# Optimization experiments

Measured on AMD Instinct MI355X. Metric: run time of the kernel, lower is better.

The kernel has to match this reference:

```python
import jax, jax.numpy as jnp
import numpy as np

T, H, I, E, TOPK = 4096, 2048, 4096, 8, 2


def setup_inputs() -> dict:
    key = jax.random.key(0)
    k0, k1, k2, k3, k4, k5 = jax.random.split(key, 6)
    return {
        "hidden_states": jax.random.normal(k0, (T, H), dtype=jnp.float32),
        "expert_affinities": jax.random.uniform(k1, (T, E), dtype=jnp.float32),
        "expert_index": jax.random.randint(k2, (T, TOPK), 0, E),
        "w_gate": jax.random.normal(k3, (E, H, I), dtype=jnp.float32) / np.float32(np.sqrt(H)),
        "w_up": jax.random.normal(k4, (E, H, I), dtype=jnp.float32) / np.float32(np.sqrt(H)),
        "w_down": jax.random.normal(k5, (E, I, H), dtype=jnp.float32) / np.float32(np.sqrt(I)),
    }


def reference(hidden_states, expert_affinities, expert_index, w_gate, w_up, w_down):
    num_experts = w_gate.shape[0]
    # top_k-hot mask (T, E); duplicate expert picks accumulate, matching torch loop
    expert_mask = jnp.sum(jax.nn.one_hot(expert_index, num_experts, dtype=jnp.float32), axis=1)
    # mask affinities to chosen experts, then L1-normalize (F.normalize p=1, eps=1e-12)
    aff = jnp.where(expert_mask == 0, 0.0, expert_affinities)
    aff = aff / jnp.maximum(jnp.sum(jnp.abs(aff), axis=1, keepdims=True), 1e-12)
    # all-experts GLU MLP: every expert processes all tokens
    g = jnp.einsum('th,ehi->eti', hidden_states, w_gate)   # (E, T, I)
    u = jnp.einsum('th,ehi->eti', hidden_states, w_up)     # (E, T, I)
    h = jax.nn.silu(g) * u                                  # (E, T, I)
    out_e = jnp.einsum('eti,eih->eth', h, w_down)           # (E, T, H)
    # affinity-weighted combine across experts
    return jnp.einsum('eth,te->th', out_e, aff)             # (T, H)
```

## Files before the change

### kernel.cpp

```cpp
#include <hip/hip_runtime.h>
#include <hip/hip_bf16.h>


constexpr int kT   = 4096;
constexpr int kH   = 2048;
constexpr int kI   = 4096;
constexpr int kE   = 8;
constexpr int kCap = 4096;
constexpr int kRowsCap = 10240;

typedef __attribute__((ext_vector_type(8))) short bf16x8;
typedef __attribute__((ext_vector_type(4))) float f32x4;

constexpr size_t HSB_OFF  = 0;
constexpr size_t HBUF_OFF = 16777216;
constexpr size_t RA_OFF   = HBUF_OFF + (size_t)kRowsCap * kI * 2;
constexpr size_t RB_OFF   = RA_OFF + (size_t)kE * kH * kI * 2;
constexpr size_t CNT_OFF  = RB_OFF + (size_t)kE * kH * kI * 2;
constexpr size_t OFF_OFF  = CNT_OFF + 256;
constexpr size_t LTOK_OFF = OFF_OFF + 256;
constexpr size_t LW_OFF   = LTOK_OFF + (size_t)kE * kCap * 4;
constexpr size_t POS_OFF  = LW_OFF + (size_t)kE * kCap * 4;
constexpr size_t WROW_OFF = POS_OFF + (size_t)kT * 2 * 4;

__device__ __forceinline__ unsigned short f2bf(float x) {
  unsigned int u = __float_as_uint(x);
  u += 0x7FFFu + ((u >> 16) & 1u);
  return (unsigned short)(u >> 16);
}
__device__ __forceinline__ unsigned pk2(float a, float b) {
  return (unsigned)f2bf(a) | ((unsigned)f2bf(b) << 16);
}
__device__ __forceinline__ float silu_f(float x) { return x / (1.f + __expf(-x)); }

__device__ __forceinline__ void async_copy16(void* lds, const void* g) {
  __builtin_amdgcn_global_load_lds(
      (const __attribute__((address_space(1))) void*)g,
      (__attribute__((address_space(3))) void*)lds, 16, 0, 0);
}

#define MFMA_BF16 __builtin_amdgcn_mfma_f32_16x16x32_bf16

__global__ void cvt_hs_kernel(const float* __restrict__ in, unsigned short* __restrict__ out) {
  size_t i = ((size_t)blockIdx.x * 256 + threadIdx.x) * 8;
  float4 a = *(const float4*)(in + i);
  float4 b = *(const float4*)(in + i + 4);
  uint4 v;
  v.x = pk2(a.x, a.y); v.y = pk2(a.z, a.w);
  v.z = pk2(b.x, b.y); v.w = pk2(b.z, b.w);
  *(uint4*)(out + i) = v;
}

__global__ __launch_bounds__(256)
void tcvt_kernel(const float* __restrict__ src, unsigned short* __restrict__ dst,
                 int K, int N) {
  __shared__ __attribute__((aligned(16))) unsigned short s[64][72];
  const size_t mat = (size_t)K * N;
  const float* S = src + (size_t)blockIdx.z * mat;
  unsigned short* D = dst + (size_t)blockIdx.z * mat;
  const int k0 = blockIdx.y * 64, n0 = blockIdx.x * 64;
  const int t  = threadIdx.x;
  const int n4 = (t & 15) * 4;
  const int k4 = (t >> 4) * 4;
  const float* p0 = S + (size_t)(k0 + k4) * N + n0 + n4;
  float4 r0 = *(const float4*)(p0);
  float4 r1 = *(const float4*)(p0 + N);
  float4 r2 = *(const float4*)(p0 + 2 * (size_t)N);
  float4 r3 = *(const float4*)(p0 + 3 * (size_t)N);
  uint2 v;
  v.x = pk2(r0.x, r1.x); v.y = pk2(r2.x, r3.x); *(uint2*)(&s[n4 + 0][k4]) = v;
  v.x = pk2(r0.y, r1.y); v.y = pk2(r2.y, r3.y); *(uint2*)(&s[n4 + 1][k4]) = v;
  v.x = pk2(r0.z, r1.z); v.y = pk2(r2.z, r3.z); *(uint2*)(&s[n4 + 2][k4]) = v;
  v.x = pk2(r0.w, r1.w); v.y = pk2(r2.w, r3.w); *(uint2*)(&s[n4 + 3][k4]) = v;
  __syncthreads();
  const int nn = t >> 3;
  const int kc = (t & 7) * 8;
#pragma unroll
  for (int i = 0; i < 2; ++i) {
    const int n = nn + i * 32;
    uint4 u = *(const uint4*)(&s[n][kc]);
    *(uint4*)(D + (size_t)(n0 + n) * K + k0 + kc) = u;
  }
}

__global__ void route_kernel(const float* __restrict__ aff, const int* __restrict__ idx,
                             int* counts, int* ltok, float* lw, int* pos) {
  int t = blockIdx.x * 256 + threadIdx.x;
  if (t >= kT) return;
  int e0 = idx[t * 2 + 0];
  int e1 = idx[t * 2 + 1];
  float a0 = aff[t * kE + e0];
  float a1 = aff[t * kE + e1];
  if (e0 == e1) {
    float w = a0 / fmaxf(fabsf(a0), 1e-12f);
    int s = atomicAdd(&counts[e0], 1);
    ltok[e0 * kCap + s] = t;
    lw[e0 * kCap + s]   = w;
    pos[t * 2 + 0] = (e0 << 12) | s;
    pos[t * 2 + 1] = -1;
  } else {
    float d = fmaxf(fabsf(a0) + fabsf(a1), 1e-12f);
    int s0 = atomicAdd(&counts[e0], 1);
    ltok[e0 * kCap + s0] = t;
    lw[e0 * kCap + s0]   = a0 / d;
    int s1 = atomicAdd(&counts[e1], 1);
    ltok[e1 * kCap + s1] = t;
    lw[e1 * kCap + s1]   = a1 / d;
    pos[t * 2 + 0] = (e0 << 12) | s0;
    pos[t * 2 + 1] = (e1 << 12) | s1;
  }
}

__global__ void prefix_kernel(const int* __restrict__ counts, int* offs) {
  if (threadIdx.x == 0 && blockIdx.x == 0) {
    int acc = 0;
    for (int e = 0; e < kE; ++e) { offs[e] = acc; acc += (counts[e] + 255) & ~255; }
  }
}

__global__ void wrow_kernel(const int* __restrict__ counts, const int* __restrict__ offs,
                            const float* __restrict__ lw, float* __restrict__ wrow) {
  int idx = blockIdx.x * 256 + threadIdx.x;
  int e = idx >> 12, s = idx & 4095;
  int cnt = counts[e];
  int al  = (cnt + 255) & ~255;
  if (s < al) wrow[offs[e] + s] = (s < cnt) ? lw[e * kCap + s] : 0.f;
}

__global__ __launch_bounds__(512, 2)
void gemm_gu_kernel(const unsigned short* __restrict__ hsb,
                    const unsigned short* __restrict__ wgT,
                    const unsigned short* __restrict__ wuT,
                    const int* __restrict__ counts, const int* __restrict__ offs,
                    const int* __restrict__ ltok, const float* __restrict__ wrow,
                    unsigned short* __restrict__ hbuf) {
  constexpr int S = kH / 32;
  __shared__ __attribute__((aligned(16))) unsigned short lds[4 * 16384];

  const int e   = blockIdx.z;
  const int cnt = counts[e];
  const int m0  = blockIdx.y * 256;
  if (m0 >= cnt) return;
  const int n0   = blockIdx.x * 128;
  const int tid  = threadIdx.x;
  const int lane = tid & 63;
  const int wv   = tid >> 6;
  const int wm   = wv >> 2;
  const int wn   = wv & 3;
  const int baseRow = offs[e] + m0;

  const int skof = ((tid & 3) ^ ((tid >> 3) & 3)) * 8;
  int sl0 = m0 + (tid >> 2);        sl0 = sl0 < cnt ? sl0 : cnt - 1;
  int sl1 = m0 + 128 + (tid >> 2);  sl1 = sl1 < cnt ? sl1 : cnt - 1;
  const unsigned short* aP0 = hsb + (size_t)ltok[e * kCap + sl0] * kH + skof;
  const unsigned short* aP1 = hsb + (size_t)ltok[e * kCap + sl1] * kH + skof;
  const unsigned short* wgP = wgT + (size_t)e * kI * kH
                                  + (size_t)(n0 + (tid >> 2)) * kH + skof;
  const unsigned short* wuP = wuT + (size_t)e * kI * kH
                                  + (size_t)(n0 + (tid >> 2)) * kH + skof;
  char* ldsb = (char*)lds;
  const int aO0 = tid * 16;
  const int aO1 = aO0 + 8192;
  const int wO  = tid * 16;

#define GU_STG_A(s) { const int sb_ = ((s) & 3) * 32768; const int ko_ = (s) * 32;  \
    async_copy16(ldsb + sb_ + aO0, aP0 + ko_);                                      \
    async_copy16(ldsb + sb_ + aO1, aP1 + ko_); }
#define GU_STG_W(s) { const int sb_ = ((s) & 3) * 32768; const int ko_ = (s) * 32;  \
    async_copy16(ldsb + sb_ + 16384 + wO, wgP + ko_);                               \
    async_copy16(ldsb + sb_ + 24576 + wO, wuP + ko_); }

  f32x4 accG[8][2] = {};
  f32x4 accU[8][2] = {};
  const int ar = lane & 15;
  const int fo = (((lane >> 4) ^ ((lane >> 1) & 3)) << 4);

#define GU_SLICE(s, STG, VM)                                                         \
  {                                                                                  \
    const char* sb = ldsb + ((s) & 3) * 32768;                                       \
    if (STG) { GU_STG_A((s) + 3); GU_STG_W((s) + 3); }                               \
    bf16x8 fA[8], fWg[2], fWu[2];                                                    \
    _Pragma("unroll") for (int mf = 0; mf < 8; ++mf)                                 \
      fA[mf] = *(const bf16x8*)(sb + (wm * 128 + mf * 16 + ar) * 64 + fo);           \
    _Pragma("unroll") for (int nf = 0; nf < 2; ++nf) {                               \
      fWg[nf] = *(const bf16x8*)(sb + 16384 + (wn * 32 + nf * 16 + ar) * 64 + fo);   \
      fWu[nf] = *(const bf16x8*)(sb + 24576 + (wn * 32 + nf * 16 + ar) * 64 + fo);   \
    }                                                                                \
    __builtin_amdgcn_s_setprio(1);                                                   \
    _Pragma("unroll") for (int mf = 0; mf < 8; ++mf)                                 \
      _Pragma("unroll") for (int nf = 0; nf < 2; ++nf) {                             \
        accG[mf][nf] = MFMA_BF16(fWg[nf], fA[mf], accG[mf][nf], 0, 0, 0);            \
        accU[mf][nf] = MFMA_BF16(fWu[nf], fA[mf], accU[mf][nf], 0, 0, 0);            \
      }                                                                              \
    __builtin_amdgcn_s_setprio(0);                                                   \
    if ((VM) >= 0) {                                                                 \
      asm volatile("s_waitcnt vmcnt(%0)" :: "i"((VM) < 0 ? 0 : (VM)) : "memory");    \
      __builtin_amdgcn_s_barrier();                                                  \
    }                                                                                \
  }

  GU_STG_A(0); GU_STG_W(0);
  GU_STG_A(1); GU_STG_W(1);
  GU_STG_A(2); GU_STG_W(2);
  asm volatile("s_waitcnt vmcnt(8)" ::: "memory");
  __builtin_amdgcn_s_barrier();

  for (int s = 0; s < S - 3; ++s) GU_SLICE(s, true, 8);
  GU_SLICE(S - 3, false, 4);
  GU_SLICE(S - 2, false, 0);
  GU_SLICE(S - 1, false, -1);
#undef GU_SLICE
#undef GU_STG_A
#undef GU_STG_W

  const int lr4 = (lane >> 4) * 4;
#pragma unroll
  for (int mf = 0; mf < 8; ++mf) {
    const int grow = baseRow + wm * 128 + mf * 16 + ar;
    const float wf = wrow[grow];
#pragma unroll
    for (int nf = 0; nf < 2; ++nf) {
      const int n = n0 + wn * 32 + nf * 16 + lr4;
      f32x4 g = accG[mf][nf], u = accU[mf][nf];
      float h0 = silu_f(g[0]) * u[0] * wf;
      float h1 = silu_f(g[1]) * u[1] * wf;
      float h2 = silu_f(g[2]) * u[2] * wf;
      float h3 = silu_f(g[3]) * u[3] * wf;
      uint2 v;
      v.x = pk2(h0, h1);
      v.y = pk2(h2, h3);
      *(uint2*)(hbuf + ((size_t)grow * kI + n)) = v;
    }
  }
}

__global__ __launch_bounds__(512, 2)
void gemm_dn_kernel(const unsigned short* __restrict__ hbuf,
                    const unsigned short* __restrict__ wdT,
                    const int* __restrict__ counts, const int* __restrict__ offs,
                    float* __restrict__ obuf) {
  constexpr int S = kI / 32;
  __shared__ __attribute__((aligned(16))) unsigned short lds[4 * 16384];

  const int e   = blockIdx.z;
  const int cnt = counts[e];
  const int m0  = blockIdx.y * 256;
  if (m0 >= cnt) return;
  const int n0   = blockIdx.x * 256;
  const int tid  = threadIdx.x;
  const int lane = tid & 63;
  const int wv   = tid >> 6;
  const int wm   = wv >> 2;
  const int wn   = wv & 3;
  const int baseRow = offs[e] + m0;

  const int skof = ((tid & 3) ^ ((tid >> 3) & 3)) * 8;
  const unsigned short* aP0 = hbuf + (size_t)(baseRow + (tid >> 2)) * kI + skof;
  const unsigned short* aP1 = hbuf + (size_t)(baseRow + 128 + (tid >> 2)) * kI + skof;
  const unsigned short* wP0 = wdT + (size_t)e * kH * kI
                                  + (size_t)(n0 + (tid >> 2)) * kI + skof;
  const unsigned short* wP1 = wdT + (size_t)e * kH * kI
                                  + (size_t)(n0 + 128 + (tid >> 2)) * kI + skof;
  char* ldsb = (char*)lds;
  const int cO0 = tid * 16;
  const int cO1 = cO0 + 8192;

#define DN_STG_A(s) { const int sb_ = ((s) & 3) * 32768; const int ko_ = (s) * 32;  \
    async_copy16(ldsb + sb_ + cO0, aP0 + ko_);                                      \
    async_copy16(ldsb + sb_ + cO1, aP1 + ko_); }
#define DN_STG_W(s) { const int sb_ = ((s) & 3) * 32768; const int ko_ = (s) * 32;  \
    async_copy16(ldsb + sb_ + 16384 + cO0, wP0 + ko_);                              \
    async_copy16(ldsb + sb_ + 16384 + cO1, wP1 + ko_); }

  f32x4 acc[8][4] = {};
  const int ar = lane & 15;
  const int fo = (((lane >> 4) ^ ((lane >> 1) & 3)) << 4);

#define DN_SLICE(s, STG, VM)                                                         \
  {                                                                                  \
    const char* sb = ldsb + ((s) & 3) * 32768;                                       \
    if (STG) { DN_STG_A((s) + 3); DN_STG_W((s) + 3); }                               \
    bf16x8 fA[8], fW[4];                                                             \
    _Pragma("unroll") for (int mf = 0; mf < 8; ++mf)                                 \
      fA[mf] = *(const bf16x8*)(sb + (wm * 128 + mf * 16 + ar) * 64 + fo);           \
    _Pragma("unroll") for (int nf = 0; nf < 4; ++nf)                                 \
      fW[nf] = *(const bf16x8*)(sb + 16384 + (wn * 64 + nf * 16 + ar) * 64 + fo);    \
    __builtin_amdgcn_s_setprio(1);                                                   \
    _Pragma("unroll") for (int mf = 0; mf < 8; ++mf)                                 \
      _Pragma("unroll") for (int nf = 0; nf < 4; ++nf)                               \
        acc[mf][nf] = MFMA_BF16(fW[nf], fA[mf], acc[mf][nf], 0, 0, 0);               \
    __builtin_amdgcn_s_setprio(0);                                                   \
    if ((VM) >= 0) {                                                                 \
      asm volatile("s_waitcnt vmcnt(%0)" :: "i"((VM) < 0 ? 0 : (VM)) : "memory");    \
      __builtin_amdgcn_s_barrier();                                                  \
    }                                                                                \
  }

  DN_STG_A(0); DN_STG_W(0);
  DN_STG_A(1); DN_STG_W(1);
  DN_STG_A(2); DN_STG_W(2);
  asm volatile("s_waitcnt vmcnt(8)" ::: "memory");
  __builtin_amdgcn_s_barrier();

  for (int s = 0; s < S - 3; ++s) DN_SLICE(s, true, 8);
  DN_SLICE(S - 3, false, 4);
  DN_SLICE(S - 2, false, 0);
  DN_SLICE(S - 1, false, -1);
#undef DN_SLICE
#undef DN_STG_A
#undef DN_STG_W

  const int lr4 = (lane >> 4) * 4;
#pragma unroll
  for (int mf = 0; mf < 8; ++mf) {
    const int grow = baseRow + wm * 128 + mf * 16 + ar;
#pragma unroll
    for (int nf = 0; nf < 4; ++nf) {
      const int n = n0 + wn * 64 + nf * 16 + lr4;
      *(f32x4*)(obuf + (size_t)grow * kH + n) = acc[mf][nf];
    }
  }
}

__global__ void combine_kernel(const float* __restrict__ obuf,
                               const int* __restrict__ pos,
                               const int* __restrict__ offs,
                               float* __restrict__ out) {
  const int t   = blockIdx.y;
  const int col = blockIdx.x * 1024 + threadIdx.x * 4;
  const int c0  = pos[t * 2 + 0];
  const int c1  = pos[t * 2 + 1];
  const int row0 = offs[c0 >> 12] + (c0 & 4095);
  float4 v = *(const float4*)(obuf + (size_t)row0 * kH + col);
  if (c1 >= 0) {
    const int row1 = offs[c1 >> 12] + (c1 & 4095);
    float4 w = *(const float4*)(obuf + (size_t)row1 * kH + col);
    v.x += w.x; v.y += w.y; v.z += w.z; v.w += w.w;
  }
  *(float4*)(out + (size_t)t * kH + col) = v;
}

extern "C" void kernel_launch(void* const* d_in, const int* in_sizes, int n_in,
                              void* d_out, int out_size, void* d_ws, size_t ws_size,
                              hipStream_t stream) {
  const float* hs   = (const float*)d_in[0];
  const float* aff  = (const float*)d_in[1];
  const int*   eidx = (const int*)d_in[2];
  const float* wg   = (const float*)d_in[3];
  const float* wu   = (const float*)d_in[4];
  const float* wd   = (const float*)d_in[5];
  float* out = (float*)d_out;

  char* ws = (char*)d_ws;
  unsigned short* hsb  = (unsigned short*)(ws + HSB_OFF);
  unsigned short* hbuf = (unsigned short*)(ws + HBUF_OFF);
  unsigned short* wgT  = (unsigned short*)(ws + RA_OFF);
  unsigned short* wdT  = (unsigned short*)(ws + RA_OFF);
  unsigned short* wuT  = (unsigned short*)(ws + RB_OFF);
  float*          obuf = (float*)(ws + RB_OFF);
  int*            cnts = (int*)(ws + CNT_OFF);
  int*            offs = (int*)(ws + OFF_OFF);
  int*            ltok = (int*)(ws + LTOK_OFF);
  float*          lwgt = (float*)(ws + LW_OFF);
  int*            pos  = (int*)(ws + POS_OFF);
  float*          wrow = (float*)(ws + WROW_OFF);

  hipMemsetAsync(cnts, 0, kE * sizeof(int), stream);

  cvt_hs_kernel<<<(kT * kH) / (256 * 8), 256, 0, stream>>>(hs, hsb);
  route_kernel<<<kT / 256, 256, 0, stream>>>(aff, eidx, cnts, ltok, lwgt, pos);
  prefix_kernel<<<1, 64, 0, stream>>>(cnts, offs);
  wrow_kernel<<<(kE * kCap) / 256, 256, 0, stream>>>(cnts, offs, lwgt, wrow);

  tcvt_kernel<<<dim3(kI / 64, kH / 64, kE), 256, 0, stream>>>(wg, wgT, kH, kI);
  tcvt_kernel<<<dim3(kI / 64, kH / 64, kE), 256, 0, stream>>>(wu, wuT, kH, kI);

  gemm_gu_kernel<<<dim3(kI / 128, kCap / 256, kE), 512, 0, stream>>>(
      hsb, wgT, wuT, cnts, offs, ltok, wrow, hbuf);

  tcvt_kernel<<<dim3(kH / 64, kI / 64, kE), 256, 0, stream>>>(wd, wdT, kI, kH);

  gemm_dn_kernel<<<dim3(kH / 256, kCap / 256, kE), 512, 0, stream>>>(
      hbuf, wdT, cnts, offs, obuf);

  combine_kernel<<<dim3(kH / 1024, kT), 256, 0, stream>>>(obuf, pos, offs, out);
}
```

Baseline: 775.9 us.

## Double-buffer A-fragment LDS reads across K slices in GEMM kernels

Both grouped GEMM kernels now read the next slice's activation fragments from LDS into a second register set while the current slice's MFMAs run, ping-ponging between two register arrays. To make the next buffer ready one slice early, the global-load waits are tightened to leave fewer copies in flight (vmcnt 4 instead of 8), and an lgkmcnt(0) wait is added before each barrier. This hides LDS read latency behind matrix math, at the cost of more vector registers (which may lower occupancy) and a shallower effective prefetch depth for global loads. The loop is unrolled by two and assumes S is even and at least 4.

```diff
diff --git a/kernel.cpp b/kernel.cpp
--- a/kernel.cpp
+++ b/kernel.cpp
@@ -175,26 +175,29 @@
   const int ar = lane & 15;
   const int fo = (((lane >> 4) ^ ((lane >> 1) & 3)) << 4);
 
-#define GU_SLICE(s, STG, VM)                                                         \
+#define GU_BODY(s, CUR, NXT, STG, RD, VM)                                            \
   {                                                                                  \
-    const char* sb = ldsb + ((s) & 3) * 32768;                                       \
+    const char* sbc = ldsb + ((s) & 3) * 32768;                                      \
+    const char* sbn = ldsb + (((s) + 1) & 3) * 32768;                                \
     if (STG) { GU_STG_A((s) + 3); GU_STG_W((s) + 3); }                               \
-    bf16x8 fA[8], fWg[2], fWu[2];                                                    \
-    _Pragma("unroll") for (int mf = 0; mf < 8; ++mf)                                 \
-      fA[mf] = *(const bf16x8*)(sb + (wm * 128 + mf * 16 + ar) * 64 + fo);           \
+    bf16x8 wg_[2], wu_[2];                                                           \
     _Pragma("unroll") for (int nf = 0; nf < 2; ++nf) {                               \
-      fWg[nf] = *(const bf16x8*)(sb + 16384 + (wn * 32 + nf * 16 + ar) * 64 + fo);   \
-      fWu[nf] = *(const bf16x8*)(sb + 24576 + (wn * 32 + nf * 16 + ar) * 64 + fo);   \
+      wg_[nf] = *(const bf16x8*)(sbc + 16384 + (wn * 32 + nf * 16 + ar) * 64 + fo);  \
+      wu_[nf] = *(const bf16x8*)(sbc + 24576 + (wn * 32 + nf * 16 + ar) * 64 + fo);  \
+    }                                                                                \
+    if (RD) {                                                                        \
+      _Pragma("unroll") for (int mf = 0; mf < 8; ++mf)                               \
+        NXT[mf] = *(const bf16x8*)(sbn + (wm * 128 + mf * 16 + ar) * 64 + fo);       \
     }                                                                                \
     __builtin_amdgcn_s_setprio(1);                                                   \
     _Pragma("unroll") for (int mf = 0; mf < 8; ++mf)                                 \
       _Pragma("unroll") for (int nf = 0; nf < 2; ++nf) {                             \
-        accG[mf][nf] = MFMA_BF16(fWg[nf], fA[mf], accG[mf][nf], 0, 0, 0);            \
-        accU[mf][nf] = MFMA_BF16(fWu[nf], fA[mf], accU[mf][nf], 0, 0, 0);            \
+        accG[mf][nf] = MFMA_BF16(wg_[nf], CUR[mf], accG[mf][nf], 0, 0, 0);           \
+        accU[mf][nf] = MFMA_BF16(wu_[nf], CUR[mf], accU[mf][nf], 0, 0, 0);           \
       }                                                                              \
     __builtin_amdgcn_s_setprio(0);                                                   \
     if ((VM) >= 0) {                                                                 \
-      asm volatile("s_waitcnt vmcnt(%0)" :: "i"((VM) < 0 ? 0 : (VM)) : "memory");    \
+      asm volatile("s_waitcnt vmcnt(%0) lgkmcnt(0)" :: "i"((VM) < 0 ? 0 : (VM)) : "memory"); \
       __builtin_amdgcn_s_barrier();                                                  \
     }                                                                                \
   }
@@ -202,14 +205,23 @@
   GU_STG_A(0); GU_STG_W(0);
   GU_STG_A(1); GU_STG_W(1);
   GU_STG_A(2); GU_STG_W(2);
-  asm volatile("s_waitcnt vmcnt(8)" ::: "memory");
+  asm volatile("s_waitcnt vmcnt(4)" ::: "memory");
   __builtin_amdgcn_s_barrier();
 
-  for (int s = 0; s < S - 3; ++s) GU_SLICE(s, true, 8);
-  GU_SLICE(S - 3, false, 4);
-  GU_SLICE(S - 2, false, 0);
-  GU_SLICE(S - 1, false, -1);
-#undef GU_SLICE
+  bf16x8 aA[8], aB[8];
+#pragma unroll
+  for (int mf = 0; mf < 8; ++mf)
+    aA[mf] = *(const bf16x8*)(ldsb + (wm * 128 + mf * 16 + ar) * 64 + fo);
+
+  for (int s = 0; s < S - 4; s += 2) {
+    GU_BODY(s,     aA, aB, 1, 1, 4);
+    GU_BODY(s + 1, aB, aA, 1, 1, 4);
+  }
+  GU_BODY(S - 4, aA, aB, 1, 1, 4);
+  GU_BODY(S - 3, aB, aA, 0, 1, 0);
+  GU_BODY(S - 2, aA, aB, 0, 1, -1);
+  GU_BODY(S - 1, aB, aA, 0, 0, -1);
+#undef GU_BODY
 #undef GU_STG_A
 #undef GU_STG_W
 
@@ -276,22 +288,25 @@
   const int ar = lane & 15;
   const int fo = (((lane >> 4) ^ ((lane >> 1) & 3)) << 4);
 
-#define DN_SLICE(s, STG, VM)                                                         \
+#define DN_BODY(s, CUR, NXT, STG, RD, VM)                                            \
   {                                                                                  \
-    const char* sb = ldsb + ((s) & 3) * 32768;                                       \
+    const char* sbc = ldsb + ((s) & 3) * 32768;                                      \
+    const char* sbn = ldsb + (((s) + 1) & 3) * 32768;                                \
     if (STG) { DN_STG_A((s) + 3); DN_STG_W((s) + 3); }                               \
-    bf16x8 fA[8], fW[4];                                                             \
-    _Pragma("unroll") for (int mf = 0; mf < 8; ++mf)                                 \
-      fA[mf] = *(const bf16x8*)(sb + (wm * 128 + mf * 16 + ar) * 64 + fo);           \
+    bf16x8 fW[4];                                                                    \
     _Pragma("unroll") for (int nf = 0; nf < 4; ++nf)                                 \
-      fW[nf] = *(const bf16x8*)(sb + 16384 + (wn * 64 + nf * 16 + ar) * 64 + fo);    \
+      fW[nf] = *(const bf16x8*)(sbc + 16384 + (wn * 64 + nf * 16 + ar) * 64 + fo);   \
+    if (RD) {                                                                        \
+      _Pragma("unroll") for (int mf = 0; mf < 8; ++mf)                               \
+        NXT[mf] = *(const bf16x8*)(sbn + (wm * 128 + mf * 16 + ar) * 64 + fo);       \
+    }                                                                                \
     __builtin_amdgcn_s_setprio(1);                                                   \
     _Pragma("unroll") for (int mf = 0; mf < 8; ++mf)                                 \
       _Pragma("unroll") for (int nf = 0; nf < 4; ++nf)                               \
-        acc[mf][nf] = MFMA_BF16(fW[nf], fA[mf], acc[mf][nf], 0, 0, 0);               \
+        acc[mf][nf] = MFMA_BF16(fW[nf], CUR[mf], acc[mf][nf], 0, 0, 0);              \
     __builtin_amdgcn_s_setprio(0);                                                   \
     if ((VM) >= 0) {                                                                 \
-      asm volatile("s_waitcnt vmcnt(%0)" :: "i"((VM) < 0 ? 0 : (VM)) : "memory");    \
+      asm volatile("s_waitcnt vmcnt(%0) lgkmcnt(0)" :: "i"((VM) < 0 ? 0 : (VM)) : "memory"); \
       __builtin_amdgcn_s_barrier();                                                  \
     }                                                                                \
   }
@@ -299,14 +314,23 @@
   DN_STG_A(0); DN_STG_W(0);
   DN_STG_A(1); DN_STG_W(1);
   DN_STG_A(2); DN_STG_W(2);
-  asm volatile("s_waitcnt vmcnt(8)" ::: "memory");
+  asm volatile("s_waitcnt vmcnt(4)" ::: "memory");
   __builtin_amdgcn_s_barrier();
 
-  for (int s = 0; s < S - 3; ++s) DN_SLICE(s, true, 8);
-  DN_SLICE(S - 3, false, 4);
-  DN_SLICE(S - 2, false, 0);
-  DN_SLICE(S - 1, false, -1);
-#undef DN_SLICE
+  bf16x8 aA[8], aB[8];
+#pragma unroll
+  for (int mf = 0; mf < 8; ++mf)
+    aA[mf] = *(const bf16x8*)(ldsb + (wm * 128 + mf * 16 + ar) * 64 + fo);
+
+  for (int s = 0; s < S - 4; s += 2) {
+    DN_BODY(s,     aA, aB, 1, 1, 4);
+    DN_BODY(s + 1, aB, aA, 1, 1, 4);
+  }
+  DN_BODY(S - 4, aA, aB, 1, 1, 4);
+  DN_BODY(S - 3, aB, aA, 0, 1, 0);
+  DN_BODY(S - 2, aA, aB, 0, 1, -1);
+  DN_BODY(S - 1, aB, aA, 0, 0, -1);
+#undef DN_BODY
 #undef DN_STG_A
 #undef DN_STG_W
 
```

Result: no change. 774.9 us (-0.1%).

## Restructure MoE GEMMs to double-buffered 64-wide K tiles with ping-pong barrier schedule

Applied to the files above, without the earlier changes.

Both the gate/up and down-projection GEMM kernels switch from a 4-stage ring of 32-wide K slices to two 64-wide K-tile buffers. Each tile is split into four MFMA quarter phases separated by barriers, with global-to-LDS async copies for later tiles issued between phases. The LDS swizzle is widened to 8 chunks and the warp-to-row mapping changes to two 128-row halves. The aim is to halve the waitcnt/barrier overhead per K unit and interleave loads with MFMA work more finely, at the cost of more barriers per tile and shallower prefetch depth.

```diff
diff --git a/kernel.cpp b/kernel.cpp
--- a/kernel.cpp
+++ b/kernel.cpp
@@ -134,8 +134,8 @@
                     const int* __restrict__ counts, const int* __restrict__ offs,
                     const int* __restrict__ ltok, const float* __restrict__ wrow,
                     unsigned short* __restrict__ hbuf) {
-  constexpr int S = kH / 32;
-  __shared__ __attribute__((aligned(16))) unsigned short lds[4 * 16384];
+  constexpr int NT = kH / 64;
+  __shared__ __attribute__((aligned(16))) unsigned short lds[2 * 32768];
 
   const int e   = blockIdx.z;
   const int cnt = counts[e];
@@ -149,89 +149,127 @@
   const int wn   = wv & 3;
   const int baseRow = offs[e] + m0;
 
-  const int skof = ((tid & 3) ^ ((tid >> 3) & 3)) * 8;
-  int sl0 = m0 + (tid >> 2);        sl0 = sl0 < cnt ? sl0 : cnt - 1;
-  int sl1 = m0 + 128 + (tid >> 2);  sl1 = sl1 < cnt ? sl1 : cnt - 1;
-  const unsigned short* aP0 = hsb + (size_t)ltok[e * kCap + sl0] * kH + skof;
-  const unsigned short* aP1 = hsb + (size_t)ltok[e * kCap + sl1] * kH + skof;
-  const unsigned short* wgP = wgT + (size_t)e * kI * kH
-                                  + (size_t)(n0 + (tid >> 2)) * kH + skof;
-  const unsigned short* wuP = wuT + (size_t)e * kI * kH
-                                  + (size_t)(n0 + (tid >> 2)) * kH + skof;
+  const int skof = ((tid & 7) ^ ((tid >> 3) & 7)) * 8;
+  const int r_   = tid >> 3;
+  int s0 = m0 + r_;        s0 = s0 < cnt ? s0 : cnt - 1;
+  int s1 = m0 + 64 + r_;   s1 = s1 < cnt ? s1 : cnt - 1;
+  int s2 = m0 + 128 + r_;  s2 = s2 < cnt ? s2 : cnt - 1;
+  int s3 = m0 + 192 + r_;  s3 = s3 < cnt ? s3 : cnt - 1;
+  const unsigned short* aP0 = hsb + (size_t)ltok[e * kCap + s0] * kH + skof;
+  const unsigned short* aP1 = hsb + (size_t)ltok[e * kCap + s1] * kH + skof;
+  const unsigned short* aP2 = hsb + (size_t)ltok[e * kCap + s2] * kH + skof;
+  const unsigned short* aP3 = hsb + (size_t)ltok[e * kCap + s3] * kH + skof;
+  const unsigned short* wgP0 = wgT + (size_t)e * kI * kH + (size_t)(n0 + r_) * kH + skof;
+  const unsigned short* wgP1 = wgT + (size_t)e * kI * kH + (size_t)(n0 + 64 + r_) * kH + skof;
+  const unsigned short* wuP0 = wuT + (size_t)e * kI * kH + (size_t)(n0 + r_) * kH + skof;
+  const unsigned short* wuP1 = wuT + (size_t)e * kI * kH + (size_t)(n0 + 64 + r_) * kH + skof;
+
   char* ldsb = (char*)lds;
-  const int aO0 = tid * 16;
-  const int aO1 = aO0 + 8192;
-  const int wO  = tid * 16;
-
-#define GU_STG_A(s) { const int sb_ = ((s) & 3) * 32768; const int ko_ = (s) * 32;  \
-    async_copy16(ldsb + sb_ + aO0, aP0 + ko_);                                      \
-    async_copy16(ldsb + sb_ + aO1, aP1 + ko_); }
-#define GU_STG_W(s) { const int sb_ = ((s) & 3) * 32768; const int ko_ = (s) * 32;  \
-    async_copy16(ldsb + sb_ + 16384 + wO, wgP + ko_);                               \
-    async_copy16(ldsb + sb_ + 24576 + wO, wuP + ko_); }
+  const int stO0 = tid * 16;
+  const int stO1 = tid * 16 + 8192;
+  const int ar  = lane & 15;
+  const int lg  = lane >> 4;
+  const int sk0 = ((lg ^ (lane & 7)) << 4);
+  const int sk1 = (((4 + lg) ^ (lane & 7)) << 4);
 
   f32x4 accG[8][2] = {};
   f32x4 accU[8][2] = {};
-  const int ar = lane & 15;
-  const int fo = (((lane >> 4) ^ ((lane >> 1) & 3)) << 4);
-
-#define GU_SLICE(s, STG, VM)                                                         \
-  {                                                                                  \
-    const char* sb = ldsb + ((s) & 3) * 32768;                                       \
-    if (STG) { GU_STG_A((s) + 3); GU_STG_W((s) + 3); }                               \
-    bf16x8 fA[8], fWg[2], fWu[2];                                                    \
-    _Pragma("unroll") for (int mf = 0; mf < 8; ++mf)                                 \
-      fA[mf] = *(const bf16x8*)(sb + (wm * 128 + mf * 16 + ar) * 64 + fo);           \
-    _Pragma("unroll") for (int nf = 0; nf < 2; ++nf) {                               \
-      fWg[nf] = *(const bf16x8*)(sb + 16384 + (wn * 32 + nf * 16 + ar) * 64 + fo);   \
-      fWu[nf] = *(const bf16x8*)(sb + 24576 + (wn * 32 + nf * 16 + ar) * 64 + fo);   \
-    }                                                                                \
-    __builtin_amdgcn_s_setprio(1);                                                   \
-    _Pragma("unroll") for (int mf = 0; mf < 8; ++mf)                                 \
-      _Pragma("unroll") for (int nf = 0; nf < 2; ++nf) {                             \
-        accG[mf][nf] = MFMA_BF16(fWg[nf], fA[mf], accG[mf][nf], 0, 0, 0);            \
-        accU[mf][nf] = MFMA_BF16(fWu[nf], fA[mf], accU[mf][nf], 0, 0, 0);            \
-      }                                                                              \
-    __builtin_amdgcn_s_setprio(0);                                                   \
-    if ((VM) >= 0) {                                                                 \
-      asm volatile("s_waitcnt vmcnt(%0)" :: "i"((VM) < 0 ? 0 : (VM)) : "memory");    \
-      __builtin_amdgcn_s_barrier();                                                  \
-    }                                                                                \
-  }
-
-  GU_STG_A(0); GU_STG_W(0);
-  GU_STG_A(1); GU_STG_W(1);
-  GU_STG_A(2); GU_STG_W(2);
-  asm volatile("s_waitcnt vmcnt(8)" ::: "memory");
-  __builtin_amdgcn_s_barrier();
-
-  for (int s = 0; s < S - 3; ++s) GU_SLICE(s, true, 8);
-  GU_SLICE(S - 3, false, 4);
-  GU_SLICE(S - 2, false, 0);
-  GU_SLICE(S - 1, false, -1);
-#undef GU_SLICE
-#undef GU_STG_A
-#undef GU_STG_W
-
-  const int lr4 = (lane >> 4) * 4;
-#pragma unroll
-  for (int mf = 0; mf < 8; ++mf) {
-    const int grow = baseRow + wm * 128 + mf * 16 + ar;
-    const float wf = wrow[grow];
-#pragma unroll
-    for (int nf = 0; nf < 2; ++nf) {
-      const int n = n0 + wn * 32 + nf * 16 + lr4;
-      f32x4 g = accG[mf][nf], u = accU[mf][nf];
-      float h0 = silu_f(g[0]) * u[0] * wf;
-      float h1 = silu_f(g[1]) * u[1] * wf;
-      float h2 = silu_f(g[2]) * u[2] * wf;
-      float h3 = silu_f(g[3]) * u[3] * wf;
-      uint2 v;
-      v.x = pk2(h0, h1);
-      v.y = pk2(h2, h3);
-      *(uint2*)(hbuf + ((size_t)grow * kI + n)) = v;
+  bf16x8 a0[4][2], a1[4][2], wgf[2][2], wuf[2][2];
+
+#define STG2(dst, p0, p1, tt) {                                   \
+    async_copy16((dst) + stO0, (p0) + (size_t)(tt) * 64);         \
+    async_copy16((dst) + stO1, (p1) + (size_t)(tt) * 64); }
+#define RD_A(dst, base, mh) _Pragma("unroll")                                  \
+  for (int mf = 0; mf < 4; ++mf) {                                             \
+    const char* rp_ = (base) + ((mh) * 128 + wm * 64 + mf * 16 + ar) * 128;    \
+    dst[mf][0] = *(const bf16x8*)(rp_ + sk0);                                  \
+    dst[mf][1] = *(const bf16x8*)(rp_ + sk1); }
+#define RD_W(dst, base) _Pragma("unroll")                                      \
+  for (int nf = 0; nf < 2; ++nf) {                                             \
+    const char* rp_ = (base) + (wn * 32 + nf * 16 + ar) * 128;                 \
+    dst[nf][0] = *(const bf16x8*)(rp_ + sk0);                                  \
+    dst[nf][1] = *(const bf16x8*)(rp_ + sk1); }
+#define MMA16(ACC, W, A, MH)                                                   \
+  __builtin_amdgcn_s_setprio(1);                                               \
+  _Pragma("unroll") for (int mf = 0; mf < 4; ++mf)                             \
+    _Pragma("unroll") for (int nf = 0; nf < 2; ++nf) {                         \
+      ACC[(MH)*4+mf][nf] = MFMA_BF16(W[nf][0], A[mf][0], ACC[(MH)*4+mf][nf], 0, 0, 0); \
+      ACC[(MH)*4+mf][nf] = MFMA_BF16(W[nf][1], A[mf][1], ACC[(MH)*4+mf][nf], 0, 0, 0); \
+    }                                                                          \
+  __builtin_amdgcn_s_setprio(0);
+
+#define GU_TILE(t, SA1, SM, VM)                                                \
+  {                                                                            \
+    char* bc = ldsb + ((t) & 1) * 65536;                                       \
+    char* bo = ldsb + (((t) + 1) & 1) * 65536;                                 \
+    RD_A(a0, bc, 0); RD_W(wgf, bc + 32768);                                    \
+    if (SA1) STG2(bo + 16384, aP2, aP3, (t) + 1);                              \
+    __builtin_amdgcn_s_barrier();                                              \
+    MMA16(accG, wgf, a0, 0);                                                   \
+    __builtin_amdgcn_s_barrier();                                              \
+    RD_W(wuf, bc + 49152);                                                     \
+    if (SM) STG2(bc, aP0, aP1, (t) + 2);                                       \
+    __builtin_amdgcn_s_barrier();                                              \
+    MMA16(accU, wuf, a0, 0);                                                   \
+    __builtin_amdgcn_s_barrier();                                              \
+    RD_A(a1, bc, 1);                                                           \
+    if (SM) STG2(bc + 32768, wgP0, wgP1, (t) + 2);                             \
+    __builtin_amdgcn_s_barrier();                                              \
+    MMA16(accG, wgf, a1, 1);                                                   \
+    __builtin_amdgcn_s_barrier();                                              \
+    if (SM) STG2(bc + 49152, wuP0, wuP1, (t) + 2);                             \
+    __builtin_amdgcn_s_barrier();                                              \
+    MMA16(accU, wuf, a1, 1);                                                   \
+    if ((VM) >= 0) {                                                           \
+      asm volatile("s_waitcnt vmcnt(%0)" :: "i"((VM) < 0 ? 0 : (VM)) : "memory"); \
+      __builtin_amdgcn_s_barrier();                                            \
+    }                                                                          \
+  }
+
+  {
+    char* b0 = ldsb;
+    char* b1 = ldsb + 65536;
+    STG2(b0,         aP0, aP1, 0);
+    STG2(b0 + 16384, aP2, aP3, 0);
+    STG2(b0 + 32768, wgP0, wgP1, 0);
+    STG2(b0 + 49152, wuP0, wuP1, 0);
+    STG2(b1,         aP0, aP1, 1);
+    STG2(b1 + 32768, wgP0, wgP1, 1);
+    STG2(b1 + 49152, wuP0, wuP1, 1);
+    asm volatile("s_waitcnt vmcnt(6)" ::: "memory");
+    __builtin_amdgcn_s_barrier();
+  }
+
+  for (int t = 0; t < NT - 2; ++t) GU_TILE(t, 1, 1, 6);
+  GU_TILE(NT - 2, 1, 0, 0);
+  GU_TILE(NT - 1, 0, 0, -1);
+#undef GU_TILE
+
+  const int lr4 = lg * 4;
+#pragma unroll
+  for (int mh = 0; mh < 2; ++mh)
+#pragma unroll
+    for (int mf = 0; mf < 4; ++mf) {
+      const int grow = baseRow + mh * 128 + wm * 64 + mf * 16 + ar;
+      const float wf = wrow[grow];
+#pragma unroll
+      for (int nf = 0; nf < 2; ++nf) {
+        const int n = n0 + wn * 32 + nf * 16 + lr4;
+        f32x4 g = accG[mh * 4 + mf][nf], u = accU[mh * 4 + mf][nf];
+        float h0 = silu_f(g[0]) * u[0] * wf;
+        float h1 = silu_f(g[1]) * u[1] * wf;
+        float h2 = silu_f(g[2]) * u[2] * wf;
+        float h3 = silu_f(g[3]) * u[3] * wf;
+        uint2 v;
+        v.x = pk2(h0, h1);
+        v.y = pk2(h2, h3);
+        *(uint2*)(hbuf + ((size_t)grow * kI + n)) = v;
+      }
     }
-  }
+#undef STG2
+#undef RD_A
+#undef RD_W
+#undef MMA16
 }
 
 __global__ __launch_bounds__(512, 2)
@@ -239,8 +277,8 @@
                     const unsigned short* __restrict__ wdT,
                     const int* __restrict__ counts, const int* __restrict__ offs,
                     float* __restrict__ obuf) {
-  constexpr int S = kI / 32;
-  __shared__ __attribute__((aligned(16))) unsigned short lds[4 * 16384];
+  constexpr int NT = kI / 64;
+  __shared__ __attribute__((aligned(16))) unsigned short lds[2 * 32768];
 
   const int e   = blockIdx.z;
   const int cnt = counts[e];
@@ -254,72 +292,116 @@
   const int wn   = wv & 3;
   const int baseRow = offs[e] + m0;
 
-  const int skof = ((tid & 3) ^ ((tid >> 3) & 3)) * 8;
-  const unsigned short* aP0 = hbuf + (size_t)(baseRow + (tid >> 2)) * kI + skof;
-  const unsigned short* aP1 = hbuf + (size_t)(baseRow + 128 + (tid >> 2)) * kI + skof;
-  const unsigned short* wP0 = wdT + (size_t)e * kH * kI
-                                  + (size_t)(n0 + (tid >> 2)) * kI + skof;
-  const unsigned short* wP1 = wdT + (size_t)e * kH * kI
-                                  + (size_t)(n0 + 128 + (tid >> 2)) * kI + skof;
+  const int skof = ((tid & 7) ^ ((tid >> 3) & 7)) * 8;
+  const int r_   = tid >> 3;
+  const unsigned short* aP0 = hbuf + (size_t)(baseRow + r_) * kI + skof;
+  const unsigned short* aP1 = hbuf + (size_t)(baseRow + 64 + r_) * kI + skof;
+  const unsigned short* aP2 = hbuf + (size_t)(baseRow + 128 + r_) * kI + skof;
+  const unsigned short* aP3 = hbuf + (size_t)(baseRow + 192 + r_) * kI + skof;
+  const unsigned short* wB = wdT + (size_t)e * kH * kI;
+  const unsigned short* wP0 = wB + (size_t)(n0 + r_) * kI + skof;
+  const unsigned short* wP1 = wB + (size_t)(n0 + 64 + r_) * kI + skof;
+  const unsigned short* wP2 = wB + (size_t)(n0 + 128 + r_) * kI + skof;
+  const unsigned short* wP3 = wB + (size_t)(n0 + 192 + r_) * kI + skof;
+
   char* ldsb = (char*)lds;
-  const int cO0 = tid * 16;
-  const int cO1 = cO0 + 8192;
-
-#define DN_STG_A(s) { const int sb_ = ((s) & 3) * 32768; const int ko_ = (s) * 32;  \
-    async_copy16(ldsb + sb_ + cO0, aP0 + ko_);                                      \
-    async_copy16(ldsb + sb_ + cO1, aP1 + ko_); }
-#define DN_STG_W(s) { const int sb_ = ((s) & 3) * 32768; const int ko_ = (s) * 32;  \
-    async_copy16(ldsb + sb_ + 16384 + cO0, wP0 + ko_);                              \
-    async_copy16(ldsb + sb_ + 16384 + cO1, wP1 + ko_); }
+  const int stO0 = tid * 16;
+  const int stO1 = tid * 16 + 8192;
+  const int ar  = lane & 15;
+  const int lg  = lane >> 4;
+  const int sk0 = ((lg ^ (lane & 7)) << 4);
+  const int sk1 = (((4 + lg) ^ (lane & 7)) << 4);
 
   f32x4 acc[8][4] = {};
-  const int ar = lane & 15;
-  const int fo = (((lane >> 4) ^ ((lane >> 1) & 3)) << 4);
-
-#define DN_SLICE(s, STG, VM)                                                         \
-  {                                                                                  \
-    const char* sb = ldsb + ((s) & 3) * 32768;                                       \
-    if (STG) { DN_STG_A((s) + 3); DN_STG_W((s) + 3); }                               \
-    bf16x8 fA[8], fW[4];                                                             \
-    _Pragma("unroll") for (int mf = 0; mf < 8; ++mf)                                 \
-      fA[mf] = *(const bf16x8*)(sb + (wm * 128 + mf * 16 + ar) * 64 + fo);           \
-    _Pragma("unroll") for (int nf = 0; nf < 4; ++nf)                                 \
-      fW[nf] = *(const bf16x8*)(sb + 16384 + (wn * 64 + nf * 16 + ar) * 64 + fo);    \
-    __builtin_amdgcn_s_setprio(1);                                                   \
-    _Pragma("unroll") for (int mf = 0; mf < 8; ++mf)                                 \
-      _Pragma("unroll") for (int nf = 0; nf < 4; ++nf)                               \
-        acc[mf][nf] = MFMA_BF16(fW[nf], fA[mf], acc[mf][nf], 0, 0, 0);               \
-    __builtin_amdgcn_s_setprio(0);                                                   \
-    if ((VM) >= 0) {                                                                 \
-      asm volatile("s_waitcnt vmcnt(%0)" :: "i"((VM) < 0 ? 0 : (VM)) : "memory");    \
-      __builtin_amdgcn_s_barrier();                                                  \
-    }                                                                                \
-  }
-
-  DN_STG_A(0); DN_STG_W(0);
-  DN_STG_A(1); DN_STG_W(1);
-  DN_STG_A(2); DN_STG_W(2);
-  asm volatile("s_waitcnt vmcnt(8)" ::: "memory");
-  __builtin_amdgcn_s_barrier();
-
-  for (int s = 0; s < S - 3; ++s) DN_SLICE(s, true, 8);
-  DN_SLICE(S - 3, false, 4);
-  DN_SLICE(S - 2, false, 0);
-  DN_SLICE(S - 1, false, -1);
-#undef DN_SLICE
-#undef DN_STG_A
-#undef DN_STG_W
-
-  const int lr4 = (lane >> 4) * 4;
-#pragma unroll
-  for (int mf = 0; mf < 8; ++mf) {
-    const int grow = baseRow + wm * 128 + mf * 16 + ar;
-#pragma unroll
-    for (int nf = 0; nf < 4; ++nf) {
-      const int n = n0 + wn * 64 + nf * 16 + lr4;
-      *(f32x4*)(obuf + (size_t)grow * kH + n) = acc[mf][nf];
+  bf16x8 a0[4][2], a1[4][2], w0[2][2], w1[2][2];
+
+#define STG2(dst, p0, p1, tt) {                                   \
+    async_copy16((dst) + stO0, (p0) + (size_t)(tt) * 64);         \
+    async_copy16((dst) + stO1, (p1) + (size_t)(tt) * 64); }
+#define RD_A(dst, base, mh) _Pragma("unroll")                                  \
+  for (int mf = 0; mf < 4; ++mf) {                                             \
+    const char* rp_ = (base) + ((mh) * 128 + wm * 64 + mf * 16 + ar) * 128;    \
+    dst[mf][0] = *(const bf16x8*)(rp_ + sk0);                                  \
+    dst[mf][1] = *(const bf16x8*)(rp_ + sk1); }
+#define RD_WN(dst, base, nh) _Pragma("unroll")                                 \
+  for (int nf = 0; nf < 2; ++nf) {                                             \
+    const char* rp_ = (base) + ((nh) * 128 + wn * 32 + nf * 16 + ar) * 128;    \
+    dst[nf][0] = *(const bf16x8*)(rp_ + sk0);                                  \
+    dst[nf][1] = *(const bf16x8*)(rp_ + sk1); }
+#define MMA16(W, A, MH, NH)                                                    \
+  __builtin_amdgcn_s_setprio(1);                                               \
+  _Pragma("unroll") for (int mf = 0; mf < 4; ++mf)                             \
+    _Pragma("unroll") for (int nf = 0; nf < 2; ++nf) {                         \
+      acc[(MH)*4+mf][(NH)*2+nf] = MFMA_BF16(W[nf][0], A[mf][0], acc[(MH)*4+mf][(NH)*2+nf], 0, 0, 0); \
+      acc[(MH)*4+mf][(NH)*2+nf] = MFMA_BF16(W[nf][1], A[mf][1], acc[(MH)*4+mf][(NH)*2+nf], 0, 0, 0); \
+    }                                                                          \
+  __builtin_amdgcn_s_setprio(0);
+
+#define DN_TILE(t, SA1, SM, VM)                                                \
+  {                                                                            \
+    char* bc = ldsb + ((t) & 1) * 65536;                                       \
+    char* bo = ldsb + (((t) + 1) & 1) * 65536;                                 \
+    RD_A(a0, bc, 0); RD_WN(w0, bc + 32768, 0);                                 \
+    if (SA1) STG2(bo + 16384, aP2, aP3, (t) + 1);                              \
+    __builtin_amdgcn_s_barrier();                                              \
+    MMA16(w0, a0, 0, 0);                                                       \
+    __builtin_amdgcn_s_barrier();                                              \
+    RD_WN(w1, bc + 32768, 1);                                                  \
+    if (SM) STG2(bc, aP0, aP1, (t) + 2);                                       \
+    __builtin_amdgcn_s_barrier();                                              \
+    MMA16(w1, a0, 0, 1);                                                       \
+    __builtin_amdgcn_s_barrier();                                              \
+    RD_A(a1, bc, 1);                                                           \
+    if (SM) STG2(bc + 32768, wP0, wP1, (t) + 2);                               \
+    __builtin_amdgcn_s_barrier();                                              \
+    MMA16(w0, a1, 1, 0);                                                       \
+    __builtin_amdgcn_s_barrier();                                              \
+    if (SM) STG2(bc + 49152, wP2, wP3, (t) + 2);                               \
+    __builtin_amdgcn_s_barrier();                                              \
+    MMA16(w1, a1, 1, 1);                                                       \
+    if ((VM) >= 0) {                                                           \
+      asm volatile("s_waitcnt vmcnt(%0)" :: "i"((VM) < 0 ? 0 : (VM)) : "memory"); \
+      __builtin_amdgcn_s_barrier();                                            \
+    }                                                                          \
+  }
+
+  {
+    char* b0 = ldsb;
+    char* b1 = ldsb + 65536;
+    STG2(b0,         aP0, aP1, 0);
+    STG2(b0 + 16384, aP2, aP3, 0);
+    STG2(b0 + 32768, wP0, wP1, 0);
+    STG2(b0 + 49152, wP2, wP3, 0);
+    STG2(b1,         aP0, aP1, 1);
+    STG2(b1 + 32768, wP0, wP1, 1);
+    STG2(b1 + 49152, wP2, wP3, 1);
+    asm volatile("s_waitcnt vmcnt(6)" ::: "memory");
+    __builtin_amdgcn_s_barrier();
+  }
+
+  for (int t = 0; t < NT - 2; ++t) DN_TILE(t, 1, 1, 6);
+  DN_TILE(NT - 2, 1, 0, 0);
+  DN_TILE(NT - 1, 0, 0, -1);
+#undef DN_TILE
+
+  const int lr4 = lg * 4;
+#pragma unroll
+  for (int mh = 0; mh < 2; ++mh)
+#pragma unroll
+    for (int mf = 0; mf < 4; ++mf) {
+      const int grow = baseRow + mh * 128 + wm * 64 + mf * 16 + ar;
+#pragma unroll
+      for (int nh = 0; nh < 2; ++nh)
+#pragma unroll
+        for (int nf = 0; nf < 2; ++nf) {
+          const int n = n0 + nh * 128 + wn * 32 + nf * 16 + lr4;
+          *(f32x4*)(obuf + (size_t)grow * kH + n) = acc[mh * 4 + mf][nh * 2 + nf];
+        }
     }
-  }
+#undef STG2
+#undef RD_A
+#undef RD_WN
+#undef MMA16
 }
 
 __global__ void combine_kernel(const float* __restrict__ obuf,
```

After: 754.8 us. -2.7%, faster.
